# Kernel tuning notes

Hardware: AMD Instinct MI355X
Metric: run time of the kernel (lower is better)

Reference implementation:

```python
import jax, jax.numpy as jnp
from jax import lax
import numpy as np

INPUT_SIZE = 1
HIDDEN_SIZE = 32
BATCH = 256
SEQ_LEN = 2048


def setup_inputs() -> dict:
    key = jax.random.key(0)
    kx, k1, k2, k3, k4 = jax.random.split(key, 5)
    H, I = HIDDEN_SIZE, INPUT_SIZE
    s = 1.0 / np.sqrt(H)  # torch LSTM default init: U(-1/sqrt(H), 1/sqrt(H))
    x = jax.random.normal(kx, (BATCH, SEQ_LEN, I), dtype=jnp.float32)
    W_ih = jax.random.uniform(k1, (4 * H, I), minval=-s, maxval=s, dtype=jnp.float32)
    W_hh = jax.random.uniform(k2, (4 * H, H), minval=-s, maxval=s, dtype=jnp.float32)
    b_ih = jax.random.uniform(k3, (4 * H,), minval=-s, maxval=s, dtype=jnp.float32)
    b_hh = jax.random.uniform(k4, (4 * H,), minval=-s, maxval=s, dtype=jnp.float32)
    return {"x": x, "W_ih": W_ih, "W_hh": W_hh, "b_ih": b_ih, "b_hh": b_hh}


def _lstm_last_hidden(x, W_ih, W_hh, b_ih, b_hh):
    # x: [B, T, I] (batch_first). PyTorch gate order: i, f, g, o.
    B = x.shape[0]
    H = W_hh.shape[1]
    # Precompute input contribution for all timesteps in one GEMM: [B, T, 4H]
    xg = jnp.einsum('bti,gi->btg', x, W_ih) + (b_ih + b_hh)
    xg = jnp.transpose(xg, (1, 0, 2))  # [T, B, 4H] for scan over time

    h0 = jnp.zeros((B, H), dtype=x.dtype)
    c0 = jnp.zeros((B, H), dtype=x.dtype)

    def step(carry, gx):
        h, c = carry
        gates = gx + h @ W_hh.T  # [B, 4H]
        i, f, g, o = jnp.split(gates, 4, axis=-1)
        i = jax.nn.sigmoid(i)
        f = jax.nn.sigmoid(f)
        g = jnp.tanh(g)
        o = jax.nn.sigmoid(o)
        c = f * c + i * g
        h = o * jnp.tanh(c)
        return (h, c), None

    (h_last, _c_last), _ = lax.scan(step, (h0, c0), xg)
    return h_last  # [B, H] == hidden[0] in the torch module


def reference(x, W_ih, W_hh, b_ih, b_hh):
    return _lstm_last_hidden(x, W_ih, W_hh, b_ih, b_hh)
```

## Files before the change

kernel.cpp:

```cpp
#include <hip/hip_runtime.h>

#define HSZ 32
#define TSEQ 2048
#define NBATCH 256

typedef float v2f __attribute__((ext_vector_type(2)));
typedef unsigned int v2u __attribute__((ext_vector_type(2)));

__device__ __forceinline__ v2f make2(float a, float b) {
    v2f r; r.x = a; r.y = b; return r;
}

__device__ __forceinline__ float hw_exp2(float x) {
#if __has_builtin(__builtin_amdgcn_exp2f)
    return __builtin_amdgcn_exp2f(x);
#else
    return exp2f(x);
#endif
}

__device__ __forceinline__ float hw_rcp(float x) {
#if __has_builtin(__builtin_amdgcn_rcpf)
    return __builtin_amdgcn_rcpf(x);
#else
    return 1.0f / x;
#endif
}

__device__ __forceinline__ float readlane_f(float v, int lane) {
    return __uint_as_float(__builtin_amdgcn_readlane(__float_as_uint(v), lane));
}

__device__ __forceinline__ float half_sum(float v) {
#if __has_builtin(__builtin_amdgcn_permlane32_swap)
    v2u r = __builtin_amdgcn_permlane32_swap(__float_as_uint(v), __float_as_uint(v), false, false);
    return __uint_as_float(r.x) + __uint_as_float(r.y);
#else
    return v + __shfl_xor(v, 32, 64);
#endif
}

#if __has_builtin(__builtin_elementwise_fma)
#define PKFMA(a, b, cc) __builtin_elementwise_fma((a), (b), (cc))
#else
__device__ __forceinline__ v2f PKFMA(v2f a, v2f b, v2f c) {
    return make2(fmaf(a.x, b.x, c.x), fmaf(a.y, b.y, c.y));
}
#endif

#define NL2E -1.44269504088896340736f

__global__ __launch_bounds__(64, 1) void lstm_last_kernel(
    const float* __restrict__ x,
    const float* __restrict__ W_ih,
    const float* __restrict__ W_hh,
    const float* __restrict__ b_ih,
    const float* __restrict__ b_hh,
    float* __restrict__ out)
{
    const int b    = blockIdx.x;
    const int l    = threadIdx.x;
    const int k    = l & 31;
    const int half = l >> 5;
    const int row0 = l;
    const int row1 = l + 64;

    __shared__ float x_lds[TSEQ + 4];

    const float4* xrow4 = (const float4*)(x + (size_t)b * TSEQ);
    float4* xl4 = (float4*)x_lds;
    #pragma unroll
    for (int j = 0; j < (TSEQ / 4) / 64; ++j)
        xl4[j * 64 + l] = xrow4[j * 64 + l];
    if (l == 0) x_lds[TSEQ] = 0.0f;

    const float sc0 = NL2E;
    const float sc1 = half ? NL2E : 2.0f * NL2E;

    v2f wp[HSZ];
    #pragma unroll
    for (int j = 0; j < HSZ; j += 4) {
        float4 a  = *(const float4*)(W_hh + row0 * HSZ + j);
        float4 c4 = *(const float4*)(W_hh + row1 * HSZ + j);
        wp[j]   = make2(a.x * sc0, c4.x * sc1);
        wp[j+1] = make2(a.y * sc0, c4.y * sc1);
        wp[j+2] = make2(a.z * sc0, c4.z * sc1);
        wp[j+3] = make2(a.w * sc0, c4.w * sc1);
    }
    const v2f wxp   = make2(W_ih[row0] * sc0, W_ih[row1] * sc1);
    const v2f biasp = make2((b_ih[row0] + b_hh[row0]) * sc0,
                            (b_ih[row1] + b_hh[row1]) * sc1);

    const float s1mul = half ? 1.0f : 2.0f;
    const float s1add = half ? 0.0f : -1.0f;

    float c  = 0.0f;
    float hk = 0.0f;

    __syncthreads();
    float xt = x_lds[0];

    #pragma unroll 1
    for (int t = 0; t < TSEQ; ++t) {
        float hs[HSZ];
        #pragma unroll
        for (int j = 0; j < HSZ; ++j) hs[j] = readlane_f(hk, 32 + j);

        float xt_next = x_lds[t + 1];

        v2f q0 = PKFMA(wxp, make2(xt, xt), biasp);
        v2f q1 = make2(0.f, 0.f), q2 = make2(0.f, 0.f), q3 = make2(0.f, 0.f);
        #pragma unroll
        for (int j = 0; j < HSZ; j += 4) {
            q0 = PKFMA(wp[j],   make2(hs[j],   hs[j]),   q0);
            q1 = PKFMA(wp[j+1], make2(hs[j+1], hs[j+1]), q1);
            q2 = PKFMA(wp[j+2], make2(hs[j+2], hs[j+2]), q2);
            q3 = PKFMA(wp[j+3], make2(hs[j+3], hs[j+3]), q3);
        }
        v2f r = (q0 + q1) + (q2 + q3);

        float a0 = hw_rcp(1.0f + hw_exp2(r.x));
        float a1 = fmaf(s1mul, hw_rcp(1.0f + hw_exp2(r.y)), s1add);

        float v  = a0 * (half ? c : a1);
        float cn = half_sum(v);
        c = cn;

        float th = fmaf(2.0f, hw_rcp(1.0f + hw_exp2(cn * (2.0f * NL2E))), -1.0f);
        hk = a1 * th;

        xt = xt_next;
    }

    if (half) out[b * HSZ + k] = hk;
}

extern "C" void kernel_launch(void* const* d_in, const int* in_sizes, int n_in,
                              void* d_out, int out_size, void* d_ws, size_t ws_size,
                              hipStream_t stream) {
    const float* x    = (const float*)d_in[0];
    const float* W_ih = (const float*)d_in[1];
    const float* W_hh = (const float*)d_in[2];
    const float* b_ih = (const float*)d_in[3];
    const float* b_hh = (const float*)d_in[4];
    float* out = (float*)d_out;

    lstm_last_kernel<<<NBATCH, 64, 0, stream>>>(x, W_ih, W_hh, b_ih, b_hh, out);
}
```

Baseline: 430.4 us.

## Replace per-step readlane broadcast of h with DPP/swizzle butterfly distribution

The old loop broadcast all 32 hidden values to every lane with 32 scalar readlanes each timestep. The new loop keeps h distributed across lanes and builds shuffled copies with DPP moves and one ds_swizzle. The W_hh weights are permuted per lane at load time to match that XOR pattern. It also rescales the cell state so the tanh argument needs no multiply, and broadcasts the o gate through a half_sum. This aims to cut scalar-unit serialization on the recurrence critical path, at the cost of more VALU DPP ops and trickier indexing that could be wrong.

```diff
diff --git a/kernel.cpp b/kernel.cpp
--- a/kernel.cpp
+++ b/kernel.cpp
@@ -25,10 +25,6 @@
 #else
     return 1.0f / x;
 #endif
-}
-
-__device__ __forceinline__ float readlane_f(float v, int lane) {
-    return __uint_as_float(__builtin_amdgcn_readlane(__float_as_uint(v), lane));
 }
 
 __device__ __forceinline__ float half_sum(float v) {
@@ -47,6 +43,20 @@
     return make2(fmaf(a.x, b.x, c.x), fmaf(a.y, b.y, c.y));
 }
 #endif
+
+#define DPPF(x, CTRL) \
+    __uint_as_float(__builtin_amdgcn_mov_dpp(__float_as_uint(x), (CTRL), 0xF, 0xF, true))
+
+__device__ __forceinline__ v2f dpp_pair(v2f s, int unused) { return s; }
+
+__device__ __forceinline__ int gg(int p) {
+    int v = 0;
+    if (p & 1) v ^= 1;
+    if (p & 2) v ^= 2;
+    if (p & 4) v ^= 7;
+    if (p & 8) v ^= 8;
+    return v;
+}
 
 #define NL2E -1.44269504088896340736f
 
@@ -77,62 +87,113 @@
     const float sc0 = NL2E;
     const float sc1 = half ? NL2E : 2.0f * NL2E;
 
-    v2f wp[HSZ];
+    v2f wA0p[8], wB0p[8], wA1p[8], wB1p[8];
     #pragma unroll
-    for (int j = 0; j < HSZ; j += 4) {
-        float4 a  = *(const float4*)(W_hh + row0 * HSZ + j);
-        float4 c4 = *(const float4*)(W_hh + row1 * HSZ + j);
-        wp[j]   = make2(a.x * sc0, c4.x * sc1);
-        wp[j+1] = make2(a.y * sc0, c4.y * sc1);
-        wp[j+2] = make2(a.z * sc0, c4.z * sc1);
-        wp[j+3] = make2(a.w * sc0, c4.w * sc1);
+    for (int m = 0; m < 8; ++m) {
+        int ia = k ^ gg(2*m), ib = k ^ gg(2*m + 1);
+        int ja = ia ^ 16,     jb = ib ^ 16;
+        wA0p[m] = make2(W_hh[row0*HSZ + ia] * sc0, W_hh[row0*HSZ + ib] * sc0);
+        wB0p[m] = make2(W_hh[row0*HSZ + ja] * sc0, W_hh[row0*HSZ + jb] * sc0);
+        wA1p[m] = make2(W_hh[row1*HSZ + ia] * sc1, W_hh[row1*HSZ + ib] * sc1);
+        wB1p[m] = make2(W_hh[row1*HSZ + ja] * sc1, W_hh[row1*HSZ + jb] * sc1);
     }
-    const v2f wxp   = make2(W_ih[row0] * sc0, W_ih[row1] * sc1);
-    const v2f biasp = make2((b_ih[row0] + b_hh[row0]) * sc0,
-                            (b_ih[row1] + b_hh[row1]) * sc1);
-
-    const float s1mul = half ? 1.0f : 2.0f;
-    const float s1add = half ? 0.0f : -1.0f;
-
-    float c  = 0.0f;
-    float hk = 0.0f;
+    const float wx0   = W_ih[row0] * sc0;
+    const float wx1   = W_ih[row1] * sc1;
+    const float bias0 = (b_ih[row0] + b_hh[row0]) * sc0;
+    const float bias1 = (b_ih[row1] + b_hh[row1]) * sc1;
+
+    const float s1mul = half ? 1.0f : -4.0f * NL2E;
+    const float s1add = half ? 0.0f :  2.0f * NL2E;
+
+    float cc    = 0.0f;
+    float h_own = 0.0f;
 
     __syncthreads();
     float xt = x_lds[0];
 
     #pragma unroll 1
     for (int t = 0; t < TSEQ; ++t) {
-        float hs[HSZ];
-        #pragma unroll
-        for (int j = 0; j < HSZ; ++j) hs[j] = readlane_f(hk, 32 + j);
-
+        float s0 = h_own;
+        float t0 = __uint_as_float(
+            __builtin_amdgcn_ds_swizzle(__float_as_uint(h_own), 0x401F));
         float xt_next = x_lds[t + 1];
 
-        v2f q0 = PKFMA(wxp, make2(xt, xt), biasp);
-        v2f q1 = make2(0.f, 0.f), q2 = make2(0.f, 0.f), q3 = make2(0.f, 0.f);
-        #pragma unroll
-        for (int j = 0; j < HSZ; j += 4) {
-            q0 = PKFMA(wp[j],   make2(hs[j],   hs[j]),   q0);
-            q1 = PKFMA(wp[j+1], make2(hs[j+1], hs[j+1]), q1);
-            q2 = PKFMA(wp[j+2], make2(hs[j+2], hs[j+2]), q2);
-            q3 = PKFMA(wp[j+3], make2(hs[j+3], hs[j+3]), q3);
-        }
-        v2f r = (q0 + q1) + (q2 + q3);
-
-        float a0 = hw_rcp(1.0f + hw_exp2(r.x));
-        float a1 = fmaf(s1mul, hw_rcp(1.0f + hw_exp2(r.y)), s1add);
-
-        float v  = a0 * (half ? c : a1);
+        v2f sp0 = make2(s0, DPPF(s0, 0xB1));
+        v2f sp1 = make2(DPPF(sp0.x, 0x4E),  DPPF(sp0.y, 0x4E));
+        v2f sp2 = make2(DPPF(sp0.x, 0x141), DPPF(sp0.y, 0x141));
+        v2f sp3 = make2(DPPF(sp1.x, 0x141), DPPF(sp1.y, 0x141));
+        v2f sp4 = make2(DPPF(sp0.x, 0x128), DPPF(sp0.y, 0x128));
+        v2f sp5 = make2(DPPF(sp1.x, 0x128), DPPF(sp1.y, 0x128));
+        v2f sp6 = make2(DPPF(sp2.x, 0x128), DPPF(sp2.y, 0x128));
+        v2f sp7 = make2(DPPF(sp3.x, 0x128), DPPF(sp3.y, 0x128));
+
+        v2f z = make2(0.f, 0.f);
+        v2f c00 = PKFMA(wA0p[0], sp0, make2(fmaf(wx0, xt, bias0), 0.f));
+        v2f c01 = PKFMA(wA0p[1], sp1, z);
+        v2f c02 = PKFMA(wA0p[2], sp2, z);
+        v2f c03 = PKFMA(wA0p[3], sp3, z);
+        c00 = PKFMA(wA0p[4], sp4, c00);
+        c01 = PKFMA(wA0p[5], sp5, c01);
+        c02 = PKFMA(wA0p[6], sp6, c02);
+        c03 = PKFMA(wA0p[7], sp7, c03);
+        v2f c10 = PKFMA(wA1p[0], sp0, make2(fmaf(wx1, xt, bias1), 0.f));
+        v2f c11 = PKFMA(wA1p[1], sp1, z);
+        v2f c12 = PKFMA(wA1p[2], sp2, z);
+        v2f c13 = PKFMA(wA1p[3], sp3, z);
+        c10 = PKFMA(wA1p[4], sp4, c10);
+        c11 = PKFMA(wA1p[5], sp5, c11);
+        c12 = PKFMA(wA1p[6], sp6, c12);
+        c13 = PKFMA(wA1p[7], sp7, c13);
+
+        v2f tp0 = make2(t0, DPPF(t0, 0xB1));
+        v2f tp1 = make2(DPPF(tp0.x, 0x4E),  DPPF(tp0.y, 0x4E));
+        v2f tp2 = make2(DPPF(tp0.x, 0x141), DPPF(tp0.y, 0x141));
+        v2f tp3 = make2(DPPF(tp1.x, 0x141), DPPF(tp1.y, 0x141));
+        v2f tp4 = make2(DPPF(tp0.x, 0x128), DPPF(tp0.y, 0x128));
+        v2f tp5 = make2(DPPF(tp1.x, 0x128), DPPF(tp1.y, 0x128));
+        v2f tp6 = make2(DPPF(tp2.x, 0x128), DPPF(tp2.y, 0x128));
+        v2f tp7 = make2(DPPF(tp3.x, 0x128), DPPF(tp3.y, 0x128));
+
+        c00 = PKFMA(wB0p[0], tp0, c00);
+        c01 = PKFMA(wB0p[1], tp1, c01);
+        c02 = PKFMA(wB0p[2], tp2, c02);
+        c03 = PKFMA(wB0p[3], tp3, c03);
+        c00 = PKFMA(wB0p[4], tp4, c00);
+        c01 = PKFMA(wB0p[5], tp5, c01);
+        c02 = PKFMA(wB0p[6], tp6, c02);
+        c03 = PKFMA(wB0p[7], tp7, c03);
+        c10 = PKFMA(wB1p[0], tp0, c10);
+        c11 = PKFMA(wB1p[1], tp1, c11);
+        c12 = PKFMA(wB1p[2], tp2, c12);
+        c13 = PKFMA(wB1p[3], tp3, c13);
+        c10 = PKFMA(wB1p[4], tp4, c10);
+        c11 = PKFMA(wB1p[5], tp5, c11);
+        c12 = PKFMA(wB1p[6], tp6, c12);
+        c13 = PKFMA(wB1p[7], tp7, c13);
+
+        v2f r0v = (c00 + c01) + (c02 + c03);
+        v2f r1v = (c10 + c11) + (c12 + c13);
+        float d0 = r0v.x + r0v.y;
+        float d1 = r1v.x + r1v.y;
+
+        float a0 = hw_rcp(1.0f + hw_exp2(d0));
+        float a1 = fmaf(s1mul, hw_rcp(1.0f + hw_exp2(d1)), s1add);
+
+        float asum  = half_sum(a1);
+        float o_all = half ? a1 : (asum - a1);
+
+        float v  = a0 * (half ? cc : a1);
         float cn = half_sum(v);
-        c = cn;
-
-        float th = fmaf(2.0f, hw_rcp(1.0f + hw_exp2(cn * (2.0f * NL2E))), -1.0f);
-        hk = a1 * th;
+        cc = cn;
+
+        float r2 = hw_rcp(1.0f + hw_exp2(cn));
+        float th = fmaf(-2.0f, r2, 1.0f);
+        h_own = o_all * th;
 
         xt = xt_next;
     }
 
-    if (half) out[b * HSZ + k] = hk;
+    if (half == 0) out[b * HSZ + k] = h_own;
 }
 
 extern "C" void kernel_launch(void* const* d_in, const int* in_sizes, int n_in,
```

Measured after the change: 472.4 us. 1.1x slower.

## Map two batch rows per wave with per-lane full gate computation via LDS

Applied to the files above, without the earlier changes.

Each 64-lane wave now handles two batch elements, one per half-wave, and the grid is halved. Each lane computes all four gates for one hidden unit, so the cross-half permlane reduction goes away. The broadcast of h, previously 32 scalar readlanes per step, becomes eight float4 LDS reads. A combined reciprocal trick computes two sigmoids with one rcp. The trade is four times more packed FMAs per lane on the serial per-step critical path, plus an LDS write/read round trip whose latency may cost more than the removed readlanes and permlane.

```diff
diff --git a/kernel.cpp b/kernel.cpp
--- a/kernel.cpp
+++ b/kernel.cpp
@@ -5,7 +5,6 @@
 #define NBATCH 256
 
 typedef float v2f __attribute__((ext_vector_type(2)));
-typedef unsigned int v2u __attribute__((ext_vector_type(2)));
 
 __device__ __forceinline__ v2f make2(float a, float b) {
     v2f r; r.x = a; r.y = b; return r;
@@ -27,19 +26,6 @@
 #endif
 }
 
-__device__ __forceinline__ float readlane_f(float v, int lane) {
-    return __uint_as_float(__builtin_amdgcn_readlane(__float_as_uint(v), lane));
-}
-
-__device__ __forceinline__ float half_sum(float v) {
-#if __has_builtin(__builtin_amdgcn_permlane32_swap)
-    v2u r = __builtin_amdgcn_permlane32_swap(__float_as_uint(v), __float_as_uint(v), false, false);
-    return __uint_as_float(r.x) + __uint_as_float(r.y);
-#else
-    return v + __shfl_xor(v, 32, 64);
-#endif
-}
-
 #if __has_builtin(__builtin_elementwise_fma)
 #define PKFMA(a, b, cc) __builtin_elementwise_fma((a), (b), (cc))
 #else
@@ -48,7 +34,7 @@
 }
 #endif
 
-#define NL2E -1.44269504088896340736f
+#define L2E 1.44269504088896340736f
 
 __global__ __launch_bounds__(64, 1) void lstm_last_kernel(
     const float* __restrict__ x,
@@ -58,81 +44,131 @@
     const float* __restrict__ b_hh,
     float* __restrict__ out)
 {
-    const int b    = blockIdx.x;
     const int l    = threadIdx.x;
     const int k    = l & 31;
     const int half = l >> 5;
-    const int row0 = l;
-    const int row1 = l + 64;
+    const int bA   = blockIdx.x;
+    const int bB   = blockIdx.x + (NBATCH / 2);
 
-    __shared__ float x_lds[TSEQ + 4];
+    __shared__ float x_lds[2 * TSEQ + 4];
+    __shared__ float h_lds[64];
 
-    const float4* xrow4 = (const float4*)(x + (size_t)b * TSEQ);
-    float4* xl4 = (float4*)x_lds;
-    #pragma unroll
-    for (int j = 0; j < (TSEQ / 4) / 64; ++j)
-        xl4[j * 64 + l] = xrow4[j * 64 + l];
-    if (l == 0) x_lds[TSEQ] = 0.0f;
+    {
+        const float4* xa = (const float4*)(x + (size_t)bA * TSEQ);
+        const float4* xb = (const float4*)(x + (size_t)bB * TSEQ);
+        float4* d0 = (float4*)x_lds;
+        float4* d1 = (float4*)(x_lds + TSEQ);
+        #pragma unroll
+        for (int j = 0; j < 8; ++j) {
+            d0[j * 64 + l] = xa[j * 64 + l];
+            d1[j * 64 + l] = xb[j * 64 + l];
+        }
+    }
+    h_lds[l] = 0.0f;
 
-    const float sc0 = NL2E;
-    const float sc1 = half ? NL2E : 2.0f * NL2E;
-
-    v2f wp[HSZ];
+    const float sI = -L2E;
+    const float sG = -2.0f * L2E;
+    v2f wi[16], wf[16], wg[16], wo[16];
     #pragma unroll
     for (int j = 0; j < HSZ; j += 4) {
-        float4 a  = *(const float4*)(W_hh + row0 * HSZ + j);
-        float4 c4 = *(const float4*)(W_hh + row1 * HSZ + j);
-        wp[j]   = make2(a.x * sc0, c4.x * sc1);
-        wp[j+1] = make2(a.y * sc0, c4.y * sc1);
-        wp[j+2] = make2(a.z * sc0, c4.z * sc1);
-        wp[j+3] = make2(a.w * sc0, c4.w * sc1);
+        float4 ri = *(const float4*)(W_hh + (size_t)(k     ) * HSZ + j);
+        float4 rf = *(const float4*)(W_hh + (size_t)(k + 32) * HSZ + j);
+        float4 rg = *(const float4*)(W_hh + (size_t)(k + 64) * HSZ + j);
+        float4 ro = *(const float4*)(W_hh + (size_t)(k + 96) * HSZ + j);
+        wi[j/2] = make2(ri.x * sI, ri.y * sI);  wi[j/2+1] = make2(ri.z * sI, ri.w * sI);
+        wf[j/2] = make2(rf.x * sI, rf.y * sI);  wf[j/2+1] = make2(rf.z * sI, rf.w * sI);
+        wg[j/2] = make2(rg.x * sG, rg.y * sG);  wg[j/2+1] = make2(rg.z * sG, rg.w * sG);
+        wo[j/2] = make2(ro.x * sI, ro.y * sI);  wo[j/2+1] = make2(ro.z * sI, ro.w * sI);
     }
-    const v2f wxp   = make2(W_ih[row0] * sc0, W_ih[row1] * sc1);
-    const v2f biasp = make2((b_ih[row0] + b_hh[row0]) * sc0,
-                            (b_ih[row1] + b_hh[row1]) * sc1);
+    const float wxi = W_ih[k]      * sI, wxf = W_ih[k + 32] * sI;
+    const float wxg = W_ih[k + 64] * sG, wxo = W_ih[k + 96] * sI;
+    const float bi = (b_ih[k]      + b_hh[k]     ) * sI;
+    const float bf = (b_ih[k + 32] + b_hh[k + 32]) * sI;
+    const float bg = (b_ih[k + 64] + b_hh[k + 64]) * sG;
+    const float bo = (b_ih[k + 96] + b_hh[k + 96]) * sI;
 
-    const float s1mul = half ? 1.0f : 2.0f;
-    const float s1add = half ? 0.0f : -1.0f;
+    const float GA = 4.0f * L2E, GB = -2.0f * L2E;
 
-    float c  = 0.0f;
-    float hk = 0.0f;
+    float cc = 0.0f;
+    float h  = 0.0f;
+
+    const float*  xbase = x_lds + half * TSEQ;
+    const float4* hb    = (const float4*)(h_lds + half * HSZ);
 
     __syncthreads();
-    float xt = x_lds[0];
+    float xt = xbase[0];
 
     #pragma unroll 1
     for (int t = 0; t < TSEQ; ++t) {
-        float hs[HSZ];
+        v2f hp[16];
         #pragma unroll
-        for (int j = 0; j < HSZ; ++j) hs[j] = readlane_f(hk, 32 + j);
+        for (int m = 0; m < 8; ++m) {
+            float4 v4 = hb[m];
+            hp[2*m]   = make2(v4.x, v4.y);
+            hp[2*m+1] = make2(v4.z, v4.w);
+        }
 
-        float xt_next = x_lds[t + 1];
+        float gxi = fmaf(wxi, xt, bi);
+        float gxf = fmaf(wxf, xt, bf);
+        float gxg = fmaf(wxg, xt, bg);
+        float gxo = fmaf(wxo, xt, bo);
+        float xtn = xbase[t + 1];
 
-        v2f q0 = PKFMA(wxp, make2(xt, xt), biasp);
-        v2f q1 = make2(0.f, 0.f), q2 = make2(0.f, 0.f), q3 = make2(0.f, 0.f);
+        v2f z = make2(0.f, 0.f);
+        v2f ci0 = z, ci1 = z, ci2 = z, ci3 = z;
+        v2f cf0 = z, cf1 = z, cf2 = z, cf3 = z;
+        v2f cg0 = z, cg1 = z, cg2 = z, cg3 = z;
+        v2f co0 = z, co1 = z, co2 = z, co3 = z;
         #pragma unroll
-        for (int j = 0; j < HSZ; j += 4) {
-            q0 = PKFMA(wp[j],   make2(hs[j],   hs[j]),   q0);
-            q1 = PKFMA(wp[j+1], make2(hs[j+1], hs[j+1]), q1);
-            q2 = PKFMA(wp[j+2], make2(hs[j+2], hs[j+2]), q2);
-            q3 = PKFMA(wp[j+3], make2(hs[j+3], hs[j+3]), q3);
+        for (int m = 0; m < 16; m += 4) {
+            ci0 = PKFMA(wi[m],   hp[m],   ci0);
+            ci1 = PKFMA(wi[m+1], hp[m+1], ci1);
+            ci2 = PKFMA(wi[m+2], hp[m+2], ci2);
+            ci3 = PKFMA(wi[m+3], hp[m+3], ci3);
+            cf0 = PKFMA(wf[m],   hp[m],   cf0);
+            cf1 = PKFMA(wf[m+1], hp[m+1], cf1);
+            cf2 = PKFMA(wf[m+2], hp[m+2], cf2);
+            cf3 = PKFMA(wf[m+3], hp[m+3], cf3);
+            cg0 = PKFMA(wg[m],   hp[m],   cg0);
+            cg1 = PKFMA(wg[m+1], hp[m+1], cg1);
+            cg2 = PKFMA(wg[m+2], hp[m+2], cg2);
+            cg3 = PKFMA(wg[m+3], hp[m+3], cg3);
+            co0 = PKFMA(wo[m],   hp[m],   co0);
+            co1 = PKFMA(wo[m+1], hp[m+1], co1);
+            co2 = PKFMA(wo[m+2], hp[m+2], co2);
+            co3 = PKFMA(wo[m+3], hp[m+3], co3);
         }
-        v2f r = (q0 + q1) + (q2 + q3);
+        v2f rvi = (ci0 + ci1) + (ci2 + ci3);
+        v2f rvf = (cf0 + cf1) + (cf2 + cf3);
+        v2f rvg = (cg0 + cg1) + (cg2 + cg3);
+        v2f rvo = (co0 + co1) + (co2 + co3);
+        float di  = (rvi.x + rvi.y) + gxi;
+        float df  = (rvf.x + rvf.y) + gxf;
+        float dg  = (rvg.x + rvg.y) + gxg;
+        float do_ = (rvo.x + rvo.y) + gxo;
 
-        float a0 = hw_rcp(1.0f + hw_exp2(r.x));
-        float a1 = fmaf(s1mul, hw_rcp(1.0f + hw_exp2(r.y)), s1add);
+        float ei = hw_exp2(di), ef = hw_exp2(df);
+        float eg = hw_exp2(dg), eo = hw_exp2(do_);
+        float ti = 1.0f + ei, tf = 1.0f + ef;
+        float tg = 1.0f + eg, to = 1.0f + eo;
+        float Rif = hw_rcp(ti * tf);
+        float Rgo = hw_rcp(tg * to);
+        float r_i = Rif * tf, r_f = Rif * ti;
+        float r_g = Rgo * to, r_o = Rgo * tg;
 
-        float v  = a0 * (half ? c : a1);
-        float cn = half_sum(v);
-        c = cn;
+        float inner = fmaf(GA, r_g, GB);
+        float cn = fmaf(r_f, cc, r_i * inner);
+        cc = cn;
 
-        float th = fmaf(2.0f, hw_rcp(1.0f + hw_exp2(cn * (2.0f * NL2E))), -1.0f);
-        hk = a1 * th;
+        float ec = hw_exp2(cn);
+        float rc = hw_rcp(1.0f + ec);
+        h = fmaf(-2.0f * r_o, rc, r_o);
 
-        xt = xt_next;
+        h_lds[l] = h;
+        xt = xtn;
     }
 
-    if (half) out[b * HSZ + k] = hk;
+    out[(half ? bB : bA) * HSZ + k] = h;
 }
 
 extern "C" void kernel_launch(void* const* d_in, const int* in_sizes, int n_in,
@@ -145,5 +181,5 @@
     const float* b_hh = (const float*)d_in[4];
     float* out = (float*)d_out;
 
-    lstm_last_kernel<<<NBATCH, 64, 0, stream>>>(x, W_ih, W_hh, b_ih, b_hh, out);
+    lstm_last_kernel<<<NBATCH / 2, 64, 0, stream>>>(x, W_ih, W_hh, b_ih, b_hh, out);
 }
```

After: 567.8 us. +31.9%, slower.
